# Performance work log

Hardware: AMD Instinct MI355X
Metric: run time of the kernel (lower is better)

The kernel has to match this reference:

```python
import jax, jax.numpy as jnp
import numpy as np

SPATIAL = ((100, 100), (50, 50), (25, 25), (13, 13))
STARTS = [0]
for _h, _w in SPATIAL[:-1]:
    STARTS.append(STARTS[-1] + _h * _w)
L_TOTAL = sum(h * w for h, w in SPATIAL)  # 13294
D, DFFN, NL, NH, NP = 256, 1024, 4, 8, 4
DH = D // NH
EPS = 1e-5


def _ln(x, g, b):
    mu = x.mean(-1, keepdims=True)
    var = ((x - mu) ** 2).mean(-1, keepdims=True)
    return (x - mu) * jax.lax.rsqrt(var + EPS) * g + b


def _bilinear(v_l, x, y, H, W):
    # v_l: [B,NH,H*W,DH]; x,y: [B,NH,Q*NP] pixel coords (grid_sample align_corners=False, zero padding)
    x0f = jnp.floor(x); y0f = jnp.floor(y)
    lx, ly = x - x0f, y - y0f
    x0 = x0f.astype(jnp.int32); y0 = y0f.astype(jnp.int32)
    acc = 0.0
    for dx, dy, w in ((0, 0, (1 - lx) * (1 - ly)), (1, 0, lx * (1 - ly)),
                      (0, 1, (1 - lx) * ly), (1, 1, lx * ly)):
        xi, yi = x0 + dx, y0 + dy
        valid = (xi >= 0) & (xi < W) & (yi >= 0) & (yi < H)
        idx = jnp.clip(yi, 0, H - 1) * W + jnp.clip(xi, 0, W - 1)
        g = jnp.take_along_axis(v_l, idx[..., None], axis=2)  # [B,NH,Q*NP,DH]
        acc = acc + g * (w * valid.astype(w.dtype))[..., None]
    return acc


def _msdeform(query, value_in, ref, norm_wh, Woff, boff, Wattn, battn, Wval, bval, Wout, bout):
    B, Q, _ = query.shape
    v = (value_in @ Wval + bval).reshape(B, L_TOTAL, NH, DH)
    off = (query @ Woff + boff).reshape(B, Q, NH, NL, NP, 2)
    aw = (query @ Wattn + battn).reshape(B, Q, NH, NL * NP)
    aw = jax.nn.softmax(aw, axis=-1).reshape(B, Q, NH, NL, NP)
    # normalized sampling locations in [0,1]: ref + offset / (W,H)
    loc = ref[:, :, None, :, None, :] + off / norm_wh[None, None, None, :, None, :]
    out = 0.0
    for l, (H, W) in enumerate(SPATIAL):
        s = STARTS[l]
        v_l = v[:, s:s + H * W].transpose(0, 2, 1, 3)          # [B,NH,HW,DH]
        loc_l = loc[:, :, :, l].transpose(0, 2, 1, 3, 4)       # [B,NH,Q,NP,2]
        x = (loc_l[..., 0] * W - 0.5).reshape(B, NH, Q * NP)
        y = (loc_l[..., 1] * H - 0.5).reshape(B, NH, Q * NP)
        samp = _bilinear(v_l, x, y, H, W).reshape(B, NH, Q, NP, DH)
        w_l = aw[:, :, :, l].transpose(0, 2, 1, 3)             # [B,NH,Q,NP]
        out = out + (samp * w_l[..., None]).sum(3)             # [B,NH,Q,DH]
    out = out.transpose(0, 2, 1, 3).reshape(B, Q, D)
    return out @ Wout + bout


def setup_inputs() -> dict:
    key = jax.random.key(0)
    ks = jax.random.split(key, 12)
    B = 4
    s = 0.02
    return {
        "src": jax.random.normal(ks[0], (B, L_TOTAL, D), jnp.float32),
        "pos": jax.random.normal(ks[1], (B, L_TOTAL, D), jnp.float32),
        "reference_points": jax.random.uniform(ks[2], (B, L_TOTAL, NL, 2), jnp.float32),
        "spatial_shapes": jnp.array(SPATIAL, jnp.int32),
        "level_start_index": jnp.array(STARTS, jnp.int32),
        "W_off": jax.random.normal(ks[3], (D, NH * NL * NP * 2), jnp.float32) * 0.01,
        "b_off": jax.random.normal(ks[4], (NH * NL * NP * 2,), jnp.float32) * 0.5,
        "W_attn": jax.random.normal(ks[5], (D, NH * NL * NP), jnp.float32) * s,
        "b_attn": jnp.zeros((NH * NL * NP,), jnp.float32),
        "W_val": jax.random.normal(ks[6], (D, D), jnp.float32) * s,
        "b_val": jnp.zeros((D,), jnp.float32),
        "W_out": jax.random.normal(ks[7], (D, D), jnp.float32) * s,
        "b_out": jnp.zeros((D,), jnp.float32),
        "ln_sa_g": jnp.ones((D,), jnp.float32),
        "ln_sa_b": jnp.zeros((D,), jnp.float32),
        "W1": jax.random.normal(ks[8], (D, DFFN), jnp.float32) * s,
        "b1": jnp.zeros((DFFN,), jnp.float32),
        "W2": jax.random.normal(ks[9], (DFFN, D), jnp.float32) * s,
        "b2": jnp.zeros((D,), jnp.float32),
        "ln_ff_g": jnp.ones((D,), jnp.float32),
        "ln_ff_b": jnp.zeros((D,), jnp.float32),
    }


def reference(src, pos, reference_points, spatial_shapes, level_start_index,
              W_off, b_off, W_attn, b_attn, W_val, b_val, W_out, b_out,
              ln_sa_g, ln_sa_b, W1, b1, W2, b2, ln_ff_g, ln_ff_b):
    # offset normalizer is (W, H) per level
    norm_wh = jnp.stack([spatial_shapes[:, 1], spatial_shapes[:, 0]], -1).astype(src.dtype)
    q = src + pos  # with_pos_embed
    sa = _msdeform(q, src, reference_points, norm_wh,
                   W_off, b_off, W_attn, b_attn, W_val, b_val, W_out, b_out)
    x = _ln(sa + src, ln_sa_g, ln_sa_b)          # dropout = identity (eval)
    y = jnp.maximum(x @ W1 + b1, 0.0) @ W2 + b2  # relu FFN
    return _ln(y + x, ln_ff_g, ln_ff_b)
```

## Files before the change

### kernel.cpp

```cpp
#include <hip/hip_runtime.h>
#include <hip/hip_bf16.h>

typedef __hip_bfloat16 bf16;
typedef short bf16x8 __attribute__((ext_vector_type(8)));
typedef float f32x4  __attribute__((ext_vector_type(4)));

#define ROWS 53176
#define LTOT 13294

__device__ __forceinline__ float b2f(bf16 v) { return __bfloat162float(v); }

__device__ __forceinline__ void gl2lds16(const void* g, void* l) {
    __builtin_amdgcn_global_load_lds(
        (const __attribute__((address_space(1))) unsigned*)g,
        (__attribute__((address_space(3))) unsigned*)l, 16, 0, 0);
}

template<bool RELU>
__global__ __launch_bounds__(256)
void mfma_gemm_n(const bf16* __restrict__ A, const bf16* __restrict__ Bt,
                 const float* __restrict__ bias, bf16* __restrict__ C,
                 int M, int N, int K)
{
    __shared__ __align__(16) short As[2][128 * 32];
    __shared__ __align__(16) short Bs[2][128 * 32];
    const int tid  = threadIdx.x;
    const int wave = tid >> 6, lane = tid & 63;

    const int nwg  = gridDim.x * gridDim.y;
    const int orig = blockIdx.y * gridDim.x + blockIdx.x;
    const int wgid = ((nwg & 7) == 0) ? ((orig & 7) * (nwg >> 3) + (orig >> 3)) : orig;
    const int bx = wgid % gridDim.x, by = wgid / gridDim.x;

    const int m0 = by * 128, n0 = bx * 128;
    const int lrow = lane >> 2, lcol = lane & 3;
    const int quad = lane >> 4, l15 = lane & 15;

    f32x4 acc[4][4];
#pragma unroll
    for (int i = 0; i < 4; ++i)
#pragma unroll
        for (int j = 0; j < 4; ++j) acc[i][j] = (f32x4){0.f, 0.f, 0.f, 0.f};

    const int wM = (wave >> 1) * 64, wN = (wave & 1) * 64;

    auto stage = [&](int p, int kk) {
#pragma unroll
        for (int q = 0; q < 2; ++q) {
            int rbase = wave * 32 + q * 16;
            int row = rbase + lrow;
            int sw = (lcol * 16) ^ ((row & 3) << 4);
            gl2lds16((const char*)(A  + (size_t)(m0 + row) * K + kk) + sw, &As[p][rbase * 32]);
            gl2lds16((const char*)(Bt + (size_t)(n0 + row) * K + kk) + sw, &Bs[p][rbase * 32]);
        }
    };

    auto compute = [&](int p) {
        bf16x8 af[4], bfr[4];
#pragma unroll
        for (int i = 0; i < 4; ++i) {
            int row = wM + i * 16 + l15;
            af[i] = *(const bf16x8*)((const char*)&As[p][row * 32]
                                     + ((quad * 16) ^ ((row & 3) << 4)));
        }
#pragma unroll
        for (int j = 0; j < 4; ++j) {
            int row = wN + j * 16 + l15;
            bfr[j] = *(const bf16x8*)((const char*)&Bs[p][row * 32]
                                      + ((quad * 16) ^ ((row & 3) << 4)));
        }
#pragma unroll
        for (int i = 0; i < 4; ++i)
#pragma unroll
            for (int j = 0; j < 4; ++j)
                acc[i][j] = __builtin_amdgcn_mfma_f32_16x16x32_bf16(bfr[j], af[i], acc[i][j], 0, 0, 0);
    };

    stage(0, 0);
    __syncthreads();
    int p = 0;
    for (int kk = 32; kk < K; kk += 32) {
        stage(p ^ 1, kk);
        compute(p);
        __syncthreads();
        p ^= 1;
    }
    compute(p);

    float4 b4[4];
#pragma unroll
    for (int j = 0; j < 4; ++j)
        b4[j] = *(const float4*)&bias[n0 + wN + j * 16 + quad * 4];

#pragma unroll
    for (int i = 0; i < 4; ++i) {
        int gm = m0 + wM + i * 16 + l15;
        if (gm >= M) continue;
#pragma unroll
        for (int j = 0; j < 4; ++j) {
            int gn = n0 + wN + j * 16 + quad * 4;
            union { bf16 h[4]; uint2 u2; } pk;
#pragma unroll
            for (int r = 0; r < 4; ++r) {
                float v = acc[i][j][r] + ((const float*)&b4[j])[r];
                if (RELU) v = fmaxf(v, 0.f);
                pk.h[r] = __float2bfloat16(v);
            }
            *(uint2*)&C[(size_t)gm * N + gn] = pk.u2;
        }
    }
}

template<typename OT>
__global__ __launch_bounds__(512)
void mfma_gemm_ln(const bf16* __restrict__ A, const bf16* __restrict__ Bt,
                  const float* __restrict__ bias, const bf16* __restrict__ res,
                  OT* __restrict__ C, const float* __restrict__ gam,
                  const float* __restrict__ bet, int M, int K)
{
    __shared__ __align__(16) short As[2][128 * 32];
    __shared__ __align__(16) short Bs[2][256 * 32];
    __shared__ float rsum[128], rsq[128];
    const int tid  = threadIdx.x;
    const int wave = tid >> 6, lane = tid & 63;
    const int m0 = blockIdx.x * 128;
    const int lrow = lane >> 2, lcol = lane & 3;
    const int quad = lane >> 4, l15 = lane & 15;
    if (tid < 128) { rsum[tid] = 0.f; rsq[tid] = 0.f; }

    f32x4 acc[4][4];
#pragma unroll
    for (int i = 0; i < 4; ++i)
#pragma unroll
        for (int j = 0; j < 4; ++j) acc[i][j] = (f32x4){0.f, 0.f, 0.f, 0.f};

    const int wM = (wave >> 2) * 64, wN = (wave & 3) * 64;

    auto stage = [&](int p, int kk) {
#pragma unroll
        for (int q = 0; q < 3; ++q) {
            int r = wave * 48 + q * 16;
            int sw;
            if (r < 128) {
                int row = r + lrow;
                sw = (lcol * 16) ^ ((row & 3) << 4);
                gl2lds16((const char*)(A + (size_t)(m0 + row) * K + kk) + sw, &As[p][r * 32]);
            } else {
                int rr = r - 128;
                int row = rr + lrow;
                sw = (lcol * 16) ^ ((row & 3) << 4);
                gl2lds16((const char*)(Bt + (size_t)(row) * K + kk) + sw, &Bs[p][rr * 32]);
            }
        }
    };

    auto compute = [&](int p) {
        bf16x8 af[4], bfr[4];
#pragma unroll
        for (int i = 0; i < 4; ++i) {
            int row = wM + i * 16 + l15;
            af[i] = *(const bf16x8*)((const char*)&As[p][row * 32]
                                     + ((quad * 16) ^ ((row & 3) << 4)));
        }
#pragma unroll
        for (int j = 0; j < 4; ++j) {
            int row = wN + j * 16 + l15;
            bfr[j] = *(const bf16x8*)((const char*)&Bs[p][row * 32]
                                      + ((quad * 16) ^ ((row & 3) << 4)));
        }
#pragma unroll
        for (int i = 0; i < 4; ++i)
#pragma unroll
            for (int j = 0; j < 4; ++j)
                acc[i][j] = __builtin_amdgcn_mfma_f32_16x16x32_bf16(bfr[j], af[i], acc[i][j], 0, 0, 0);
    };

    stage(0, 0);
    __syncthreads();
    int p = 0;
    for (int kk = 32; kk < K; kk += 32) {
        stage(p ^ 1, kk);
        compute(p);
        __syncthreads();
        p ^= 1;
    }
    compute(p);

    float4 b4[4], g4[4], be4[4];
#pragma unroll
    for (int j = 0; j < 4; ++j) {
        int gn = wN + j * 16 + quad * 4;
        b4[j]  = *(const float4*)&bias[gn];
        g4[j]  = *(const float4*)&gam[gn];
        be4[j] = *(const float4*)&bet[gn];
    }

    float lsum[4], lsq[4];
#pragma unroll
    for (int i = 0; i < 4; ++i) {
        int gm = m0 + wM + i * 16 + l15;
        lsum[i] = 0.f; lsq[i] = 0.f;
#pragma unroll
        for (int j = 0; j < 4; ++j) {
            int gn = wN + j * 16 + quad * 4;
            float r4[4] = {0.f, 0.f, 0.f, 0.f};
            if (gm < M) {
                uint2 ru = *(const uint2*)&res[(size_t)gm * 256 + gn];
                const bf16* rh = (const bf16*)&ru;
#pragma unroll
                for (int r = 0; r < 4; ++r) r4[r] = b2f(rh[r]);
            }
#pragma unroll
            for (int r = 0; r < 4; ++r) {
                float v = acc[i][j][r] + ((const float*)&b4[j])[r] + r4[r];
                acc[i][j][r] = v;
                lsum[i] += v;
                lsq[i]  += v * v;
            }
        }
#pragma unroll
        for (int mask = 16; mask <= 32; mask <<= 1) {
            lsum[i] += __shfl_xor(lsum[i], mask);
            lsq[i]  += __shfl_xor(lsq[i], mask);
        }
    }
    if (quad == 0) {
#pragma unroll
        for (int i = 0; i < 4; ++i) {
            atomicAdd(&rsum[wM + i * 16 + l15], lsum[i]);
            atomicAdd(&rsq [wM + i * 16 + l15], lsq[i]);
        }
    }
    __syncthreads();

#pragma unroll
    for (int i = 0; i < 4; ++i) {
        int lr = wM + i * 16 + l15;
        int gm = m0 + lr;
        if (gm >= M) continue;
        float mean = rsum[lr] * (1.f / 256.f);
        float var  = rsq[lr] * (1.f / 256.f) - mean * mean;
        float rstd = rsqrtf(fmaxf(var, 0.f) + 1e-5f);
#pragma unroll
        for (int j = 0; j < 4; ++j) {
            int gn = wN + j * 16 + quad * 4;
            if constexpr (sizeof(OT) == 2) {
                union { bf16 h[4]; uint2 u2; } pk;
#pragma unroll
                for (int r = 0; r < 4; ++r)
                    pk.h[r] = __float2bfloat16((acc[i][j][r] - mean) * rstd *
                              ((const float*)&g4[j])[r] + ((const float*)&be4[j])[r]);
                *(uint2*)&((bf16*)C)[(size_t)gm * 256 + gn] = pk.u2;
            } else {
                float4 o;
#pragma unroll
                for (int r = 0; r < 4; ++r)
                    ((float*)&o)[r] = (acc[i][j][r] - mean) * rstd *
                              ((const float*)&g4[j])[r] + ((const float*)&be4[j])[r];
                *(float4*)&((float*)C)[(size_t)gm * 256 + gn] = o;
            }
        }
    }
}

__global__ void cast_qs_kernel(const float* __restrict__ s, const float* __restrict__ p,
                               bf16* __restrict__ sb, bf16* __restrict__ qb, int n4)
{
    int i = blockIdx.x * 256 + threadIdx.x;
    if (i >= n4) return;
    float4 sv = ((const float4*)s)[i];
    float4 pv = ((const float4*)p)[i];
    union { bf16 h[4]; uint2 u; } a, b;
    a.h[0] = __float2bfloat16(sv.x); a.h[1] = __float2bfloat16(sv.y);
    a.h[2] = __float2bfloat16(sv.z); a.h[3] = __float2bfloat16(sv.w);
    b.h[0] = __float2bfloat16(sv.x + pv.x); b.h[1] = __float2bfloat16(sv.y + pv.y);
    b.h[2] = __float2bfloat16(sv.z + pv.z); b.h[3] = __float2bfloat16(sv.w + pv.w);
    ((uint2*)sb)[i] = a.u;
    ((uint2*)qb)[i] = b.u;
}

__global__ void wcast_all(const float* __restrict__ Wval, const float* __restrict__ Woff,
                          const float* __restrict__ Wattn, const float* __restrict__ Wout,
                          const float* __restrict__ W1, const float* __restrict__ W2,
                          const float* __restrict__ boff, const float* __restrict__ battn,
                          bf16* __restrict__ Wval_t, bf16* __restrict__ Wcat_t,
                          bf16* __restrict__ Wout_t, bf16* __restrict__ W1_t,
                          bf16* __restrict__ W2_t, float* __restrict__ bcat)
{
    int e = blockIdx.x * 256 + threadIdx.x;
    if (e < 384) bcat[e] = (e < 256) ? boff[e] : battn[e - 256];
    if (e < 65536) {
        int n = e >> 8, k = e & 255;
        Wval_t[e] = __float2bfloat16(Wval[k * 256 + n]);
    } else if (e < 163840) {
        int i = e - 65536; int n = i >> 8, k = i & 255;
        float w = (n < 256) ? Woff[k * 256 + n] : Wattn[k * 128 + (n - 256)];
        Wcat_t[i] = __float2bfloat16(w);
    } else if (e < 229376) {
        int i = e - 163840; int n = i >> 8, k = i & 255;
        Wout_t[i] = __float2bfloat16(Wout[k * 256 + n]);
    } else if (e < 491520) {
        int i = e - 229376; int n = i >> 8, k = i & 255;
        W1_t[i] = __float2bfloat16(W1[k * 1024 + n]);
    } else if (e < 753664) {
        int i = e - 491520; int n = i >> 10, k = i & 1023;
        W2_t[i] = __float2bfloat16(W2[k * 256 + n]);
    }
}

__global__ __launch_bounds__(256)
void sample_kernel(const bf16* __restrict__ v, const bf16* __restrict__ ocat,
                   const float* __restrict__ ref, bf16* __restrict__ samp)
{
    __shared__ int4 tab[16][33];
    const int tid = threadIdx.x;
    const int grp = tid >> 4, lane = tid & 15;
    const int gidx = blockIdx.x * 16 + grp;
    const int h = gidx & 7, bq = gidx >> 3, b = bq / LTOT;

    {
        const int p = lane, l = p >> 2, pp = p & 3;
        const int W = (l == 0) ? 100 : (l == 1) ? 50 : (l == 2) ? 25 : 13;
        const int S = (l == 0) ? 0 : (l == 1) ? 10000 : (l == 2) ? 12500 : 13125;
        const float fW = (float)W;
        float rx = ref[(size_t)bq * 8 + l * 2 + 0];
        float ry = ref[(size_t)bq * 8 + l * 2 + 1];
        const bf16* ob = ocat + (size_t)bq * 384;
        float ox = b2f(ob[h * 32 + l * 8 + pp * 2 + 0]);
        float oy = b2f(ob[h * 32 + l * 8 + pp * 2 + 1]);
        float lg = b2f(ob[256 + h * 16 + p]);
        float m = lg;
#pragma unroll
        for (int mask = 1; mask <= 8; mask <<= 1) m = fmaxf(m, __shfl_xor(m, mask));
        float ev = __expf(lg - m);
        float s = ev;
#pragma unroll
        for (int mask = 1; mask <= 8; mask <<= 1) s += __shfl_xor(s, mask);
        float wgt = ev / s;

        float x = fmaf(rx, fW, ox - 0.5f);
        float y = fmaf(ry, fW, oy - 0.5f);
        float x0f = floorf(x), y0f = floorf(y);
        float lx = x - x0f, ly = y - y0f;
        int x0 = (int)x0f, y0 = (int)y0f;
        float tw[4] = {(1.f - lx) * (1.f - ly), lx * (1.f - ly),
                       (1.f - lx) * ly,         lx * ly};
        const int base = (b * LTOT + S) * 512 + h * 64;
        int  o[4]; float w[4];
#pragma unroll
        for (int t = 0; t < 4; ++t) {
            int xi = x0 + (t & 1), yi = y0 + (t >> 1);
            bool ok = (xi >= 0) & (xi < W) & (yi >= 0) & (yi < W);
            o[t] = ok ? base + (yi * W + xi) * 512 : 0;
            w[t] = ok ? wgt * tw[t] : 0.f;
        }
        tab[grp][p * 2 + 0] = make_int4(o[0], __float_as_int(w[0]), o[1], __float_as_int(w[1]));
        tab[grp][p * 2 + 1] = make_int4(o[2], __float_as_int(w[2]), o[3], __float_as_int(w[3]));
    }
    __syncthreads();

    const int lofs = lane * 4;
    const char* vc = (const char*)v;
    float a0 = 0.f, a1 = 0.f;
#pragma unroll 4
    for (int e2 = 0; e2 < 32; ++e2) {
        int4 q = tab[grp][e2];
        unsigned u0 = *(const unsigned*)(vc + (size_t)(unsigned)(q.x + lofs));
        unsigned u1 = *(const unsigned*)(vc + (size_t)(unsigned)(q.z + lofs));
        float w0 = __int_as_float(q.y), w1 = __int_as_float(q.w);
        a0 += w0 * __uint_as_float(u0 << 16);
        a1 += w0 * __uint_as_float(u0);
        a0 += w1 * __uint_as_float(u1 << 16);
        a1 += w1 * __uint_as_float(u1);
    }
    union { struct { bf16 a, b; } h2; unsigned u; } r;
    r.h2.a = __float2bfloat16(a0);
    r.h2.b = __float2bfloat16(a1);
    *(unsigned*)((char*)samp + (size_t)gidx * 64 + lane * 4) = r.u;
}

extern "C" void kernel_launch(void* const* d_in, const int* in_sizes, int n_in,
                              void* d_out, int out_size, void* d_ws, size_t ws_size,
                              hipStream_t stream)
{
    const float* src     = (const float*)d_in[0];
    const float* pos     = (const float*)d_in[1];
    const float* ref     = (const float*)d_in[2];
    const float* W_off   = (const float*)d_in[5];
    const float* b_off   = (const float*)d_in[6];
    const float* W_attn  = (const float*)d_in[7];
    const float* b_attn  = (const float*)d_in[8];
    const float* W_val   = (const float*)d_in[9];
    const float* b_val   = (const float*)d_in[10];
    const float* W_out   = (const float*)d_in[11];
    const float* b_out   = (const float*)d_in[12];
    const float* ln_sa_g = (const float*)d_in[13];
    const float* ln_sa_b = (const float*)d_in[14];
    const float* W1      = (const float*)d_in[15];
    const float* b1      = (const float*)d_in[16];
    const float* W2      = (const float*)d_in[17];
    const float* b2      = (const float*)d_in[18];
    const float* ln_ff_g = (const float*)d_in[19];
    const float* ln_ff_b = (const float*)d_in[20];

    char* ws = (char*)d_ws;
    bf16* sb     = (bf16*)(ws);
    bf16* qb     = (bf16*)(ws + 27226112);
    bf16* samp   = (bf16*)(ws + 27226112);
    bf16* vbuf   = (bf16*)(ws + 54452224);
    bf16* ocat   = (bf16*)(ws + 81678336);
    bf16* xb16   = (bf16*)(ws + 122517504);
    bf16* hbuf   = (bf16*)(ws);
    bf16* Wval_t = (bf16*)(ws + 149743616);
    bf16* Wcat_t = (bf16*)(ws + 149874688);
    float* bcat  = (float*)(ws + 150071296);
    bf16* Wout_t = (bf16*)(ws + 150072832);
    bf16* W1_t   = (bf16*)(ws + 150203904);
    bf16* W2_t   = (bf16*)(ws + 150728192);
    float* outf  = (float*)d_out;

    dim3 blk(256);

    cast_qs_kernel<<<dim3((ROWS * 64 + 255) / 256), blk, 0, stream>>>(src, pos, sb, qb, ROWS * 64);
    wcast_all<<<dim3(2944), blk, 0, stream>>>(W_val, W_off, W_attn, W_out, W1, W2,
                                              b_off, b_attn,
                                              Wval_t, Wcat_t, Wout_t, W1_t, W2_t, bcat);

    mfma_gemm_n<false><<<dim3(2, 416), blk, 0, stream>>>(sb, Wval_t, b_val, vbuf, ROWS, 256, 256);
    mfma_gemm_n<false><<<dim3(3, 416), blk, 0, stream>>>(qb, Wcat_t, bcat, ocat, ROWS, 384, 256);
    sample_kernel<<<dim3(ROWS * 8 / 16), blk, 0, stream>>>(vbuf, ocat, ref, samp);
    mfma_gemm_ln<bf16><<<dim3(416), dim3(512), 0, stream>>>(
        samp, Wout_t, b_out, sb, xb16, ln_sa_g, ln_sa_b, ROWS, 256);
    mfma_gemm_n<true><<<dim3(8, 416), blk, 0, stream>>>(xb16, W1_t, b1, hbuf, ROWS, 1024, 256);
    mfma_gemm_ln<float><<<dim3(416), dim3(512), 0, stream>>>(
        hbuf, W2_t, b2, xb16, outf, ln_ff_g, ln_ff_b, ROWS, 1024);
}
```

Before: 475.1 us.

## Widen sampling gathers to 16-byte loads and remap blocks per XCD

The sampling kernel now handles 64 query-head pairs per block with 4 threads each instead of 16 threads each. Each thread gathers 16-byte (8 bf16) chunks per corner rather than 4-byte ones, and computes softmax and bilinear corner tables for a whole level. Block IDs are remapped so consecutive logical blocks land on the same XCD, which should improve L2 locality for neighbouring queries. The goal is fewer, wider memory transactions in this gather-bound kernel, at the cost of more registers per thread and fewer threads overall.

```diff
diff --git a/kernel.cpp b/kernel.cpp
--- a/kernel.cpp
+++ b/kernel.cpp
@@ -312,71 +312,98 @@
 void sample_kernel(const bf16* __restrict__ v, const bf16* __restrict__ ocat,
                    const float* __restrict__ ref, bf16* __restrict__ samp)
 {
-    __shared__ int4 tab[16][33];
+    __shared__ int4 tab[64][33];
     const int tid = threadIdx.x;
-    const int grp = tid >> 4, lane = tid & 15;
-    const int gidx = blockIdx.x * 16 + grp;
+
+    const int nwg = gridDim.x;
+    const int orig = blockIdx.x;
+    const int xcd = orig & 7, loc = orig >> 3;
+    const int qn = nwg >> 3, rr = nwg & 7;
+    const int bid = (xcd < rr ? xcd * (qn + 1) : rr * (qn + 1) + (xcd - rr) * qn) + loc;
+
+    const int ps = tid >> 2;
+    const int qt = tid & 3;
+    const int gidx = bid * 64 + ps;
     const int h = gidx & 7, bq = gidx >> 3, b = bq / LTOT;
 
     {
-        const int p = lane, l = p >> 2, pp = p & 3;
+        const int l = qt;
         const int W = (l == 0) ? 100 : (l == 1) ? 50 : (l == 2) ? 25 : 13;
         const int S = (l == 0) ? 0 : (l == 1) ? 10000 : (l == 2) ? 12500 : 13125;
         const float fW = (float)W;
         float rx = ref[(size_t)bq * 8 + l * 2 + 0];
         float ry = ref[(size_t)bq * 8 + l * 2 + 1];
         const bf16* ob = ocat + (size_t)bq * 384;
-        float ox = b2f(ob[h * 32 + l * 8 + pp * 2 + 0]);
-        float oy = b2f(ob[h * 32 + l * 8 + pp * 2 + 1]);
-        float lg = b2f(ob[256 + h * 16 + p]);
-        float m = lg;
-#pragma unroll
-        for (int mask = 1; mask <= 8; mask <<= 1) m = fmaxf(m, __shfl_xor(m, mask));
-        float ev = __expf(lg - m);
-        float s = ev;
-#pragma unroll
-        for (int mask = 1; mask <= 8; mask <<= 1) s += __shfl_xor(s, mask);
-        float wgt = ev / s;
-
-        float x = fmaf(rx, fW, ox - 0.5f);
-        float y = fmaf(ry, fW, oy - 0.5f);
-        float x0f = floorf(x), y0f = floorf(y);
-        float lx = x - x0f, ly = y - y0f;
-        int x0 = (int)x0f, y0 = (int)y0f;
-        float tw[4] = {(1.f - lx) * (1.f - ly), lx * (1.f - ly),
-                       (1.f - lx) * ly,         lx * ly};
+        float lg[4], ox[4], oy[4];
+#pragma unroll
+        for (int k = 0; k < 4; ++k) {
+            ox[k] = b2f(ob[h * 32 + l * 8 + k * 2 + 0]);
+            oy[k] = b2f(ob[h * 32 + l * 8 + k * 2 + 1]);
+            lg[k] = b2f(ob[256 + h * 16 + l * 4 + k]);
+        }
+        float m = fmaxf(fmaxf(lg[0], lg[1]), fmaxf(lg[2], lg[3]));
+        m = fmaxf(m, __shfl_xor(m, 1));
+        m = fmaxf(m, __shfl_xor(m, 2));
+        float ev[4]; float s = 0.f;
+#pragma unroll
+        for (int k = 0; k < 4; ++k) { ev[k] = __expf(lg[k] - m); s += ev[k]; }
+        s += __shfl_xor(s, 1);
+        s += __shfl_xor(s, 2);
+        float inv = 1.f / s;
         const int base = (b * LTOT + S) * 512 + h * 64;
-        int  o[4]; float w[4];
-#pragma unroll
-        for (int t = 0; t < 4; ++t) {
-            int xi = x0 + (t & 1), yi = y0 + (t >> 1);
-            bool ok = (xi >= 0) & (xi < W) & (yi >= 0) & (yi < W);
-            o[t] = ok ? base + (yi * W + xi) * 512 : 0;
-            w[t] = ok ? wgt * tw[t] : 0.f;
-        }
-        tab[grp][p * 2 + 0] = make_int4(o[0], __float_as_int(w[0]), o[1], __float_as_int(w[1]));
-        tab[grp][p * 2 + 1] = make_int4(o[2], __float_as_int(w[2]), o[3], __float_as_int(w[3]));
+#pragma unroll
+        for (int k = 0; k < 4; ++k) {
+            float wgt = ev[k] * inv;
+            float x = fmaf(rx, fW, ox[k] - 0.5f);
+            float y = fmaf(ry, fW, oy[k] - 0.5f);
+            float x0f = floorf(x), y0f = floorf(y);
+            float lx = x - x0f, ly = y - y0f;
+            int x0 = (int)x0f, y0 = (int)y0f;
+            float tw[4] = {(1.f - lx) * (1.f - ly), lx * (1.f - ly),
+                           (1.f - lx) * ly,         lx * ly};
+            int o[4]; float w[4];
+#pragma unroll
+            for (int t = 0; t < 4; ++t) {
+                int xi = x0 + (t & 1), yi = y0 + (t >> 1);
+                bool ok = (xi >= 0) & (xi < W) & (yi >= 0) & (yi < W);
+                o[t] = ok ? base + (yi * W + xi) * 512 : 0;
+                w[t] = ok ? wgt * tw[t] : 0.f;
+            }
+            int e = (l * 4 + k) * 2;
+            tab[ps][e + 0] = make_int4(o[0], __float_as_int(w[0]), o[1], __float_as_int(w[1]));
+            tab[ps][e + 1] = make_int4(o[2], __float_as_int(w[2]), o[3], __float_as_int(w[3]));
+        }
     }
     __syncthreads();
 
-    const int lofs = lane * 4;
+    const int lofs = qt * 16;
     const char* vc = (const char*)v;
-    float a0 = 0.f, a1 = 0.f;
-#pragma unroll 4
+    float al[4] = {0.f, 0.f, 0.f, 0.f}, ah[4] = {0.f, 0.f, 0.f, 0.f};
+#pragma unroll 8
     for (int e2 = 0; e2 < 32; ++e2) {
-        int4 q = tab[grp][e2];
-        unsigned u0 = *(const unsigned*)(vc + (size_t)(unsigned)(q.x + lofs));
-        unsigned u1 = *(const unsigned*)(vc + (size_t)(unsigned)(q.z + lofs));
+        int4 q = tab[ps][e2];
+        uint4 u0 = *(const uint4*)(vc + (size_t)(unsigned)(q.x + lofs));
+        uint4 u1 = *(const uint4*)(vc + (size_t)(unsigned)(q.z + lofs));
         float w0 = __int_as_float(q.y), w1 = __int_as_float(q.w);
-        a0 += w0 * __uint_as_float(u0 << 16);
-        a1 += w0 * __uint_as_float(u0);
-        a0 += w1 * __uint_as_float(u1 << 16);
-        a1 += w1 * __uint_as_float(u1);
-    }
-    union { struct { bf16 a, b; } h2; unsigned u; } r;
-    r.h2.a = __float2bfloat16(a0);
-    r.h2.b = __float2bfloat16(a1);
-    *(unsigned*)((char*)samp + (size_t)gidx * 64 + lane * 4) = r.u;
+#pragma unroll
+        for (int j = 0; j < 4; ++j) {
+            unsigned e0 = ((const unsigned*)&u0)[j];
+            unsigned e1 = ((const unsigned*)&u1)[j];
+            al[j] += w0 * __uint_as_float(e0 << 16);
+            ah[j] += w0 * __uint_as_float(e0);
+            al[j] += w1 * __uint_as_float(e1 << 16);
+            ah[j] += w1 * __uint_as_float(e1);
+        }
+    }
+    union { unsigned u[4]; uint4 q; } r;
+#pragma unroll
+    for (int j = 0; j < 4; ++j) {
+        union { struct { bf16 a, b; } h2; unsigned u; } t2;
+        t2.h2.a = __float2bfloat16(al[j]);
+        t2.h2.b = __float2bfloat16(ah[j]);
+        r.u[j] = t2.u;
+    }
+    *(uint4*)((char*)samp + (size_t)gidx * 64 + lofs) = r.q;
 }
 
 extern "C" void kernel_launch(void* const* d_in, const int* in_sizes, int n_in,
@@ -428,7 +455,7 @@
 
     mfma_gemm_n<false><<<dim3(2, 416), blk, 0, stream>>>(sb, Wval_t, b_val, vbuf, ROWS, 256, 256);
     mfma_gemm_n<false><<<dim3(3, 416), blk, 0, stream>>>(qb, Wcat_t, bcat, ocat, ROWS, 384, 256);
-    sample_kernel<<<dim3(ROWS * 8 / 16), blk, 0, stream>>>(vbuf, ocat, ref, samp);
+    sample_kernel<<<dim3(ROWS * 8 / 64), blk, 0, stream>>>(vbuf, ocat, ref, samp);
     mfma_gemm_ln<bf16><<<dim3(416), dim3(512), 0, stream>>>(
         samp, Wout_t, b_out, sb, xb16, ln_sa_g, ln_sa_b, ROWS, 256);
     mfma_gemm_n<true><<<dim3(8, 416), blk, 0, stream>>>(xb16, W1_t, b1, hbuf, ROWS, 1024, 256);
```

Result: no change. 468.8 us (-1.3%).
